# Optimization experiments

Hardware: AMD Instinct MI355X
Metric: run time of the kernel (lower is better)

## Reference

```python
import jax, jax.numpy as jnp
import numpy as np

N_NODES = 100000
N_EDGES = 600000
IN_DIM, HID_DIM, OUT_DIM = 128, 128, 128
NEG_SLOPE = 0.2  # PyG GATConv default


def _glorot(key, shape):
    fan = sum(shape)
    lim = jnp.sqrt(6.0 / fan)
    return jax.random.uniform(key, shape, jnp.float32, -lim, lim)


def setup_inputs() -> dict:
    key = jax.random.key(0)
    ks = jax.random.split(key, 10)
    x = jax.random.normal(ks[0], (N_NODES, IN_DIM), jnp.float32)
    edge_index = jax.random.randint(ks[1], (2, N_EDGES), 0, N_NODES, jnp.int64)
    return {
        "x": x,
        "edge_index": edge_index,
        "W1": _glorot(ks[2], (IN_DIM, HID_DIM)),
        "a_src1": _glorot(ks[3], (HID_DIM,)),
        "a_dst1": _glorot(ks[4], (HID_DIM,)),
        "b1": jnp.zeros((HID_DIM,), jnp.float32),
        "W2": _glorot(ks[5], (HID_DIM, OUT_DIM)),
        "a_src2": _glorot(ks[6], (OUT_DIM,)),
        "a_dst2": _glorot(ks[7], (OUT_DIM,)),
        "b2": jnp.zeros((OUT_DIM,), jnp.float32),
    }


def _gat_conv(x, src, dst, W, a_src, a_dst, b, n_nodes):
    """Single-head PyG-style GATConv (concat=True, heads=1, with self-loops already in src/dst)."""
    h = x @ W                                   # [N, F]
    alpha_s = h @ a_src                         # [N]
    alpha_d = h @ a_dst                         # [N]
    e = jax.nn.leaky_relu(alpha_s[src] + alpha_d[dst], NEG_SLOPE)  # [E]
    # segment softmax over incoming edges of each dst node
    m = jax.lax.stop_gradient(jax.ops.segment_max(e, dst, num_segments=n_nodes))
    w = jnp.exp(e - m[dst])                     # [E]
    denom = jax.ops.segment_sum(w, dst, num_segments=n_nodes)  # [N]
    alpha = w / denom[dst]                      # [E]
    out = jax.ops.segment_sum(h[src] * alpha[:, None], dst, num_segments=n_nodes)
    return out + b


def reference(x, edge_index, W1, a_src1, a_dst1, b1, W2, a_src2, a_dst2, b2):
    n = x.shape[0]
    loop = jnp.arange(n, dtype=edge_index.dtype)
    src = jnp.concatenate([edge_index[0], loop])  # add self-loops (PyG default)
    dst = jnp.concatenate([edge_index[1], loop])
    h = jax.nn.relu(_gat_conv(x, src, dst, W1, a_src1, a_dst1, b1, n))
    out = _gat_conv(h, src, dst, W2, a_src2, a_dst2, b2, n)
    return out.mean(axis=0)  # [out_dim]
```

## Files before the change

kernel.cpp:

```cpp
#include <hip/hip_runtime.h>


#define NEG_SLOPE 0.2f

typedef __attribute__((ext_vector_type(8))) short bf16x8;
typedef __attribute__((ext_vector_type(4))) float f32x4;

__device__ __forceinline__ float leaky(float x) { return x > 0.0f ? x : NEG_SLOPE * x; }

__device__ __forceinline__ unsigned int bf16rne(float f) {
  unsigned int u = __float_as_uint(f);
  return (u + 0x7fffu + ((u >> 16) & 1u)) >> 16;
}
__device__ __forceinline__ unsigned int packbf(float a, float b) {
  return bf16rne(a) | (bf16rne(b) << 16);
}
__device__ __forceinline__ float bf_lo(unsigned int u) { return __uint_as_float(u << 16); }
__device__ __forceinline__ float bf_hi(unsigned int u) { return __uint_as_float(u & 0xffff0000u); }

__device__ __forceinline__ void accum8(float* a, float w, uint4 h) {
  a[0] += w * bf_lo(h.x); a[1] += w * bf_hi(h.x);
  a[2] += w * bf_lo(h.y); a[3] += w * bf_hi(h.y);
  a[4] += w * bf_lo(h.z); a[5] += w * bf_hi(h.z);
  a[6] += w * bf_lo(h.w); a[7] += w * bf_hi(h.w);
}

__device__ __forceinline__ float2 gat_node2(
    const uint4* __restrict__ H4, const float* __restrict__ vas,
    const float* __restrict__ vad, const int* __restrict__ fill,
    const int* __restrict__ esrcp, const int2* __restrict__ ovf,
    const int* __restrict__ ovfn, int node0, int node1, int nclamp,
    int lane, int l, float* acc0, float* acc1, float* eself_out) {
  int t0 = esrcp[(size_t)node0 * 16 + l];
  int t1 = esrcp[(size_t)node1 * 16 + l];
  int dg0 = fill[node0];
  int dg1 = fill[node1];
  float ad0 = vad[node0], ad1 = vad[node1];
  float as0 = vas[node0], as1 = vas[node1];
  uint4 hs0 = H4[(size_t)node0 * 16 + l];
  uint4 hs1 = H4[(size_t)node1 * 16 + l];
  int u0 = min(max(t0, 0), nclamp);
  int u1 = min(max(t1, 0), nclamp);
  float vs0 = vas[u0];
  float vs1 = vas[u1];
  uint4 hb0[8], hb1[8];
#pragma unroll
  for (int i = 0; i < 8; i++) {
    int ut = __shfl(u0, (lane & 48) + i, 64);
    hb0[i] = H4[(size_t)ut * 16 + l];
  }
#pragma unroll
  for (int i = 0; i < 8; i++) {
    int ut = __shfl(u1, (lane & 48) + i, 64);
    hb1[i] = H4[(size_t)ut * 16 + l];
  }
  const bool big0 = dg0 > 8, big1 = dg1 > 8;
  uint4 hc0[8];
  if (big0) {
#pragma unroll
    for (int i = 0; i < 8; i++) {
      int ut = __shfl(u0, (lane & 48) + 8 + i, 64);
      hc0[i] = H4[(size_t)ut * 16 + l];
    }
  }
  float es0 = leaky(as0 + ad0), es1 = leaky(as1 + ad1);
  float wj0 = (l < dg0) ? __expf(leaky(vs0 + ad0) - es0) : 0.f;
  float wj1 = (l < dg1) ? __expf(leaky(vs1 + ad1) - es1) : 0.f;
  float ds0 = wj0, ds1 = wj1;
#pragma unroll
  for (int o = 8; o; o >>= 1) ds0 += __shfl_xor(ds0, o, 16);
#pragma unroll
  for (int o = 8; o; o >>= 1) ds1 += __shfl_xor(ds1, o, 16);
#pragma unroll
  for (int i = 0; i < 8; i++) {
    float w = __shfl(wj0, (lane & 48) + i, 64);
    accum8(acc0, w, hb0[i]);
  }
  if (big0) {
#pragma unroll
    for (int i = 0; i < 8; i++) {
      float w = __shfl(wj0, (lane & 48) + 8 + i, 64);
      accum8(acc0, w, hc0[i]);
    }
  }
  uint4 hc1[8];
  if (big1) {
#pragma unroll
    for (int i = 0; i < 8; i++) {
      int ut = __shfl(u1, (lane & 48) + 8 + i, 64);
      hc1[i] = H4[(size_t)ut * 16 + l];
    }
  }
#pragma unroll
  for (int i = 0; i < 8; i++) {
    float w = __shfl(wj1, (lane & 48) + i, 64);
    accum8(acc1, w, hb1[i]);
  }
  if (big1) {
#pragma unroll
    for (int i = 0; i < 8; i++) {
      float w = __shfl(wj1, (lane & 48) + 8 + i, 64);
      accum8(acc1, w, hc1[i]);
    }
  }
  if (dg0 > 16 || dg1 > 16) {
    int ovn = *ovfn;
    for (int k = 0; k < ovn; k++) {
      int2 ent = ovf[k];
      if (ent.x == node0) {
        float w = __expf(leaky(vas[ent.y] + ad0) - es0);
        ds0 += w;
        accum8(acc0, w, H4[(size_t)ent.y * 16 + l]);
      }
      if (ent.x == node1) {
        float w = __expf(leaky(vas[ent.y] + ad1) - es1);
        ds1 += w;
        accum8(acc1, w, H4[(size_t)ent.y * 16 + l]);
      }
    }
  }
  accum8(acc0, 1.0f, hs0);
  accum8(acc1, 1.0f, hs1);
  eself_out[0] = es0;
  eself_out[1] = es1;
  return make_float2(1.0f / (ds0 + 1.0f), 1.0f / (ds1 + 1.0f));
}

__global__ __launch_bounds__(256) void setup_k(const float* __restrict__ W1,
                                               const float* __restrict__ W2,
                                               unsigned short* __restrict__ Wf1,
                                               unsigned short* __restrict__ Wf2,
                                               int* __restrict__ fill,
                                               int* __restrict__ esrcp,
                                               int* __restrict__ ovfn,
                                               float* __restrict__ partial,
                                               int n, int nfb) {
  const int b = blockIdx.x;
  if (b < 2) {
    const float* W = b ? W2 : W1;
    unsigned short* Wf = b ? Wf2 : Wf1;
    for (int idx = threadIdx.x; idx < 16384; idx += 256) {
      int j = idx & 7;
      int lane = (idx >> 3) & 63;
      int fid = idx >> 9;
      int ct = fid >> 2, ks = fid & 3;
      int q = lane >> 4, l15 = lane & 15;
      Wf[idx] = (unsigned short)bf16rne(W[(ks * 32 + q * 8 + j) * 128 + ct * 16 + l15]);
    }
    return;
  }
  if (b == 2) {
    for (int i = threadIdx.x; i < 64 * 128; i += 256) partial[i] = 0.f;
    if (threadIdx.x == 0) *ovfn = 0;
    return;
  }
  if (b < 3 + nfb) {
    int base = (b - 3) * 1024 + threadIdx.x * 4;
#pragma unroll
    for (int i = 0; i < 4; i++)
      if (base + i < n) fill[base + i] = 0;
    return;
  }
  size_t base = (size_t)(b - 3 - nfb) * 1024 + threadIdx.x * 4;
  size_t tot = (size_t)n * 16;
  if (base + 4 <= tot) {
    *(int4*)&esrcp[base] = make_int4(0, 0, 0, 0);
  } else {
    for (size_t i = base; i < tot; i++) esrcp[i] = 0;
  }
}

__global__ void scatter_kernel(const int* __restrict__ src, const int* __restrict__ dst,
                               int* __restrict__ fill, int* __restrict__ esrcp,
                               int2* __restrict__ ovf, int* __restrict__ ovfn, int E) {
  int e = blockIdx.x * 256 + threadIdx.x;
  if (e < E) {
    int v = dst[e];
    int sv = src[e];
    int p = atomicAdd(&fill[v], 1);
    if (p < 16) {
      esrcp[(size_t)v * 16 + p] = sv;
    } else {
      int k = atomicAdd(ovfn, 1);
      ovf[k] = make_int2(v, sv);
    }
  }
}

__device__ __forceinline__ void cvt_f32(const float4* raw, bf16x8* xf) {
#pragma unroll
  for (int ks = 0; ks < 4; ks++) {
    union { bf16x8 v; unsigned int u[4]; } cv;
    cv.u[0] = packbf(raw[2 * ks].x, raw[2 * ks].y);
    cv.u[1] = packbf(raw[2 * ks].z, raw[2 * ks].w);
    cv.u[2] = packbf(raw[2 * ks + 1].x, raw[2 * ks + 1].y);
    cv.u[3] = packbf(raw[2 * ks + 1].z, raw[2 * ks + 1].w);
    xf[ks] = cv.v;
  }
}

__device__ __forceinline__ void mfma_tile(const unsigned short* WL, const bf16x8* xf,
                                          const float* __restrict__ a_s,
                                          const float* __restrict__ a_d,
                                          unsigned short* __restrict__ H,
                                          float* __restrict__ vas,
                                          float* __restrict__ vad, int myrow, bool act,
                                          int lane, int q) {
  f32x4 acc[8];
#pragma unroll
  for (int ct = 0; ct < 8; ct++) acc[ct] = (f32x4){0.f, 0.f, 0.f, 0.f};
#pragma unroll
  for (int ks = 0; ks < 4; ks++) {
    bf16x8 wf[8];
#pragma unroll
    for (int ct = 0; ct < 8; ct++)
      wf[ct] = *(const bf16x8*)&WL[(((ct << 2) + ks) << 9) + lane * 8];
#pragma unroll
    for (int ct = 0; ct < 8; ct++)
      acc[ct] = __builtin_amdgcn_mfma_f32_16x16x32_bf16(wf[ct], xf[ks], acc[ct], 0, 0, 0);
  }
  float ds = 0.f, dd = 0.f;
#pragma unroll
  for (int ct = 0; ct < 8; ct++) {
    const int c0 = ct * 16 + q * 4;
    float4 as4 = *(const float4*)&a_s[c0];
    float4 ad4 = *(const float4*)&a_d[c0];
    ds += acc[ct][0] * as4.x + acc[ct][1] * as4.y + acc[ct][2] * as4.z + acc[ct][3] * as4.w;
    dd += acc[ct][0] * ad4.x + acc[ct][1] * ad4.y + acc[ct][2] * ad4.z + acc[ct][3] * ad4.w;
    if (act) {
      uint2 o;
      o.x = packbf(acc[ct][0], acc[ct][1]);
      o.y = packbf(acc[ct][2], acc[ct][3]);
      *(uint2*)&H[(size_t)myrow * 128 + c0] = o;
    }
  }
  ds += __shfl_xor(ds, 16, 64);
  ds += __shfl_xor(ds, 32, 64);
  dd += __shfl_xor(dd, 16, 64);
  dd += __shfl_xor(dd, 32, 64);
  if (q == 0 && act) {
    vas[myrow] = ds;
    vad[myrow] = dd;
  }
}

__global__ __launch_bounds__(256) void gemm_mfma1(const float* __restrict__ Xf,
                                                  const unsigned short* __restrict__ Wf,
                                                  const float* __restrict__ a_s,
                                                  const float* __restrict__ a_d,
                                                  unsigned short* __restrict__ H,
                                                  float* __restrict__ vas,
                                                  float* __restrict__ vad, int n,
                                                  int nt16, int ngemm) {
  __shared__ unsigned short WL[32 * 512];
  const int lane = threadIdx.x & 63;
  const int wv = threadIdx.x >> 6;
  const int l15 = lane & 15;
  const int q = lane >> 4;
  const int t0 = blockIdx.x * 4 + wv;
  const int t1 = t0 + ngemm * 4;
  const int r0 = t0 * 16 + l15;
  const int r1 = t1 * 16 + l15;
  const bool wact0 = t0 < nt16;
  const bool wact1 = t1 < nt16;
  const bool act0 = wact0 && (r0 < n);
  const bool act1 = wact1 && (r1 < n);

  float4 raw0[8];
  if (wact0) {
#pragma unroll
    for (int ks = 0; ks < 4; ks++) {
      float4 z = {0.f, 0.f, 0.f, 0.f};
      raw0[2 * ks] = z;
      raw0[2 * ks + 1] = z;
      if (act0) {
        raw0[2 * ks] = *(const float4*)&Xf[(size_t)r0 * 128 + ks * 32 + q * 8];
        raw0[2 * ks + 1] = *(const float4*)&Xf[(size_t)r0 * 128 + ks * 32 + q * 8 + 4];
      }
    }
  }
  {
    const uint4* __restrict__ Wg4 = (const uint4*)Wf;
    uint4* WL4 = (uint4*)WL;
#pragma unroll
    for (int j = 0; j < 8; j++) WL4[threadIdx.x + 256 * j] = Wg4[threadIdx.x + 256 * j];
  }
  __syncthreads();
  if (!wact0) return;

  float4 raw1[8];
  if (wact1) {
#pragma unroll
    for (int ks = 0; ks < 4; ks++) {
      float4 z = {0.f, 0.f, 0.f, 0.f};
      raw1[2 * ks] = z;
      raw1[2 * ks + 1] = z;
      if (act1) {
        raw1[2 * ks] = *(const float4*)&Xf[(size_t)r1 * 128 + ks * 32 + q * 8];
        raw1[2 * ks + 1] = *(const float4*)&Xf[(size_t)r1 * 128 + ks * 32 + q * 8 + 4];
      }
    }
  }

  bf16x8 xf[4];
  cvt_f32(raw0, xf);
  mfma_tile(WL, xf, a_s, a_d, H, vas, vad, r0, act0, lane, q);
  if (wact1) {
    cvt_f32(raw1, xf);
    mfma_tile(WL, xf, a_s, a_d, H, vas, vad, r1, act1, lane, q);
  }
}

__global__ __launch_bounds__(256, 3) void agg1_gemm2(
    const unsigned short* __restrict__ HA, const float* __restrict__ vas1,
    const float* __restrict__ vad1, const int* __restrict__ fill,
    const int* __restrict__ esrcp, const int2* __restrict__ ovf,
    const int* __restrict__ ovfn, const float* __restrict__ b1,
    const unsigned short* __restrict__ Wf2, const float* __restrict__ a_s2,
    const float* __restrict__ a_d2, unsigned short* __restrict__ HB,
    float* __restrict__ vas2, float* __restrict__ vad2, int n) {
  __shared__ unsigned short Atile[32 * 128];
  __shared__ float sdot[2][2][4][16];
  const int tid = threadIdx.x;
  const int lane = tid & 63;
  const int wv = tid >> 6;
  const int q = lane >> 4;
  const int l = lane & 15;
  const int row = wv * 4 + q;
  const int base = blockIdx.x * 32;
  const int node0 = base + row;
  const int node1 = base + row + 16;
  const bool valid0 = node0 < n, valid1 = node1 < n;
  const int n0s = valid0 ? node0 : n - 1;
  const int n1s = valid1 ? node1 : n - 1;
  const uint4* __restrict__ H4 = (const uint4*)HA;

  float acc0[8], acc1[8];
#pragma unroll
  for (int k = 0; k < 8; k++) { acc0[k] = 0.f; acc1[k] = 0.f; }
  float es[2];
  float2 inv = gat_node2(H4, vas1, vad1, fill, esrcp, ovf, ovfn, n0s, n1s, n - 1,
                         lane, l, acc0, acc1, es);

  float4 b0 = *(const float4*)&b1[8 * l];
  float4 b1v = *(const float4*)&b1[8 * l + 4];
  uint4 o0 = {0u, 0u, 0u, 0u}, o1 = {0u, 0u, 0u, 0u};
  if (valid0) {
    float r0_ = fmaxf(acc0[0] * inv.x + b0.x, 0.f), r1_ = fmaxf(acc0[1] * inv.x + b0.y, 0.f);
    float r2_ = fmaxf(acc0[2] * inv.x + b0.z, 0.f), r3_ = fmaxf(acc0[3] * inv.x + b0.w, 0.f);
    float r4_ = fmaxf(acc0[4] * inv.x + b1v.x, 0.f), r5_ = fmaxf(acc0[5] * inv.x + b1v.y, 0.f);
    float r6_ = fmaxf(acc0[6] * inv.x + b1v.z, 0.f), r7_ = fmaxf(acc0[7] * inv.x + b1v.w, 0.f);
    o0.x = packbf(r0_, r1_); o0.y = packbf(r2_, r3_);
    o0.z = packbf(r4_, r5_); o0.w = packbf(r6_, r7_);
  }
  if (valid1) {
    float r0_ = fmaxf(acc1[0] * inv.y + b0.x, 0.f), r1_ = fmaxf(acc1[1] * inv.y + b0.y, 0.f);
    float r2_ = fmaxf(acc1[2] * inv.y + b0.z, 0.f), r3_ = fmaxf(acc1[3] * inv.y + b0.w, 0.f);
    float r4_ = fmaxf(acc1[4] * inv.y + b1v.x, 0.f), r5_ = fmaxf(acc1[5] * inv.y + b1v.y, 0.f);
    float r6_ = fmaxf(acc1[6] * inv.y + b1v.z, 0.f), r7_ = fmaxf(acc1[7] * inv.y + b1v.w, 0.f);
    o1.x = packbf(r0_, r1_); o1.y = packbf(r2_, r3_);
    o1.z = packbf(r4_, r5_); o1.w = packbf(r6_, r7_);
  }
  *(uint4*)&Atile[row * 128 + ((l ^ (row & 7)) << 3)] = o0;
  *(uint4*)&Atile[(row + 16) * 128 + ((l ^ (row & 7)) << 3)] = o1;
  __syncthreads();

  const int ct0 = 2 * wv, ct1 = 2 * wv + 1;
  f32x4 aA0 = {0.f, 0.f, 0.f, 0.f}, aB0 = aA0, aA1 = aA0, aB1 = aA0;
#pragma unroll
  for (int ks = 0; ks < 4; ks++) {
    bf16x8 w0 = *(const bf16x8*)&Wf2[(((ct0 << 2) + ks) << 9) + lane * 8];
    bf16x8 w1 = *(const bf16x8*)&Wf2[(((ct1 << 2) + ks) << 9) + lane * 8];
    bf16x8 x0 = *(const bf16x8*)&Atile[l * 128 + ((((ks << 2) + q) ^ (l & 7)) << 3)];
    bf16x8 x1 = *(const bf16x8*)&Atile[(16 + l) * 128 + ((((ks << 2) + q) ^ (l & 7)) << 3)];
    aA0 = __builtin_amdgcn_mfma_f32_16x16x32_bf16(w0, x0, aA0, 0, 0, 0);
    aB0 = __builtin_amdgcn_mfma_f32_16x16x32_bf16(w1, x0, aB0, 0, 0, 0);
    aA1 = __builtin_amdgcn_mfma_f32_16x16x32_bf16(w0, x1, aA1, 0, 0, 0);
    aB1 = __builtin_amdgcn_mfma_f32_16x16x32_bf16(w1, x1, aB1, 0, 0, 0);
  }

#pragma unroll
  for (int t = 0; t < 2; t++) {
    f32x4 aA = t ? aA1 : aA0;
    f32x4 aB = t ? aB1 : aB0;
    const int myrow = base + t * 16 + l;
    const bool ract = myrow < n;
    float ds = 0.f, dd = 0.f;
    {
      const int c0 = ct0 * 16 + q * 4;
      float4 as4 = *(const float4*)&a_s2[c0];
      float4 ad4 = *(const float4*)&a_d2[c0];
      ds += aA[0] * as4.x + aA[1] * as4.y + aA[2] * as4.z + aA[3] * as4.w;
      dd += aA[0] * ad4.x + aA[1] * ad4.y + aA[2] * ad4.z + aA[3] * ad4.w;
      if (ract) {
        uint2 ov;
        ov.x = packbf(aA[0], aA[1]);
        ov.y = packbf(aA[2], aA[3]);
        *(uint2*)&HB[(size_t)myrow * 128 + c0] = ov;
      }
    }
    {
      const int c0 = ct1 * 16 + q * 4;
      float4 as4 = *(const float4*)&a_s2[c0];
      float4 ad4 = *(const float4*)&a_d2[c0];
      ds += aB[0] * as4.x + aB[1] * as4.y + aB[2] * as4.z + aB[3] * as4.w;
      dd += aB[0] * ad4.x + aB[1] * ad4.y + aB[2] * ad4.z + aB[3] * ad4.w;
      if (ract) {
        uint2 ov;
        ov.x = packbf(aB[0], aB[1]);
        ov.y = packbf(aB[2], aB[3]);
        *(uint2*)&HB[(size_t)myrow * 128 + c0] = ov;
      }
    }
    ds += __shfl_xor(ds, 16, 64);
    ds += __shfl_xor(ds, 32, 64);
    dd += __shfl_xor(dd, 16, 64);
    dd += __shfl_xor(dd, 32, 64);
    if (q == 0) {
      sdot[t][0][wv][l] = ds;
      sdot[t][1][wv][l] = dd;
    }
  }
  __syncthreads();
  if (tid < 32) {
    int t = tid >> 4, i = tid & 15;
    int nn = base + tid;
    if (nn < n) {
      vas2[nn] = sdot[t][0][0][i] + sdot[t][0][1][i] + sdot[t][0][2][i] + sdot[t][0][3][i];
      vad2[nn] = sdot[t][1][0][i] + sdot[t][1][1][i] + sdot[t][1][2][i] + sdot[t][1][3][i];
    }
  }
}

__global__ __launch_bounds__(256, 3) void gat_agg_l2(
    const unsigned short* __restrict__ H, const float* __restrict__ vas,
    const float* __restrict__ vad, const int* __restrict__ fill,
    const int* __restrict__ esrcp, const int2* __restrict__ ovf,
    const int* __restrict__ ovfn, const float* __restrict__ bias,
    float* __restrict__ partial, int n) {
  const int tid = threadIdx.x;
  const int lane = tid & 63;
  const int wv = tid >> 6;
  const int q = lane >> 4;
  const int l = lane & 15;
  const int row = wv * 4 + q;
  const int base = blockIdx.x * 32;
  const int node0 = base + row;
  const int node1 = base + row + 16;
  const bool valid0 = node0 < n, valid1 = node1 < n;
  const int n0s = valid0 ? node0 : n - 1;
  const int n1s = valid1 ? node1 : n - 1;
  const uint4* __restrict__ H4 = (const uint4*)H;

  float acc0[8], acc1[8];
#pragma unroll
  for (int k = 0; k < 8; k++) { acc0[k] = 0.f; acc1[k] = 0.f; }
  float es[2];
  float2 inv = gat_node2(H4, vas, vad, fill, esrcp, ovf, ovfn, n0s, n1s, n - 1,
                         lane, l, acc0, acc1, es);

  float4 b0 = *(const float4*)&bias[8 * l];
  float4 b1v = *(const float4*)&bias[8 * l + 4];
  float out[8];
  const float i0 = valid0 ? inv.x : 0.f;
  const float i1 = valid1 ? inv.y : 0.f;
  const float bm = (valid0 ? 1.f : 0.f) + (valid1 ? 1.f : 0.f);
  out[0] = acc0[0] * i0 + acc1[0] * i1 + bm * b0.x;
  out[1] = acc0[1] * i0 + acc1[1] * i1 + bm * b0.y;
  out[2] = acc0[2] * i0 + acc1[2] * i1 + bm * b0.z;
  out[3] = acc0[3] * i0 + acc1[3] * i1 + bm * b0.w;
  out[4] = acc0[4] * i0 + acc1[4] * i1 + bm * b1v.x;
  out[5] = acc0[5] * i0 + acc1[5] * i1 + bm * b1v.y;
  out[6] = acc0[6] * i0 + acc1[6] * i1 + bm * b1v.z;
  out[7] = acc0[7] * i0 + acc1[7] * i1 + bm * b1v.w;

#pragma unroll
  for (int k = 0; k < 8; k++) {
    out[k] += __shfl_xor(out[k], 16, 64);
    out[k] += __shfl_xor(out[k], 32, 64);
  }
  __shared__ float red[4][128];
  if (q == 0) {
#pragma unroll
    for (int k = 0; k < 8; k++) red[wv][8 * l + k] = out[k];
  }
  __syncthreads();
  if (tid < 128) {
    float sm = red[0][tid] + red[1][tid] + red[2][tid] + red[3][tid];
    atomicAdd(&partial[(blockIdx.x & 63) * 128 + tid], sm);
  }
}

__global__ void finalize_k(const float* __restrict__ partial, float* __restrict__ out,
                           float invn) {
  int c = threadIdx.x;
  float s = 0.f;
#pragma unroll 8
  for (int r = 0; r < 64; r++) s += partial[r * 128 + c];
  out[c] = s * invn;
}

extern "C" void kernel_launch(void* const* d_in, const int* in_sizes, int n_in,
                              void* d_out, int out_size, void* d_ws, size_t ws_size,
                              hipStream_t stream) {
  const float* x = (const float*)d_in[0];
  const int* ei = (const int*)d_in[1];
  const float* W1 = (const float*)d_in[2];
  const float* a_src1 = (const float*)d_in[3];
  const float* a_dst1 = (const float*)d_in[4];
  const float* b1 = (const float*)d_in[5];
  const float* W2 = (const float*)d_in[6];
  const float* a_src2 = (const float*)d_in[7];
  const float* a_dst2 = (const float*)d_in[8];
  const float* b2 = (const float*)d_in[9];
  float* out = (float*)d_out;

  const int N = in_sizes[0] / 128;
  const int E = in_sizes[1] / 2;
  const int* src = ei;
  const int* dst = ei + E;

  const size_t rowpadded = (size_t)(N + 256) * 128;

  char* p = (char*)d_ws;
  unsigned short* HA = (unsigned short*)p; p += rowpadded * 2;
  unsigned short* HB = (unsigned short*)p; p += rowpadded * 2;
  float* vas1 = (float*)p;    p += (size_t)N * 4;
  float* vad1 = (float*)p;    p += (size_t)N * 4;
  float* vas2 = (float*)p;    p += (size_t)N * 4;
  float* vad2 = (float*)p;    p += (size_t)N * 4;
  int* fill = (int*)p;        p += (size_t)N * 4;
  int* esrcp = (int*)p;       p += (size_t)N * 16 * 4;
  int2* ovf = (int2*)p;       p += (size_t)E * 8;
  int* ovfn = (int*)p;        p += 16;
  float* partial = (float*)p; p += 64 * 128 * 4;
  unsigned short* Wf1 = (unsigned short*)p; p += 16384 * 2;
  unsigned short* Wf2 = (unsigned short*)p; p += 16384 * 2;

  const int eblocks = (E + 255) / 256;
  const int nt16 = (N + 15) / 16;
  const int ngemm = (nt16 + 7) / 8;
  const int aggblocks = (N + 31) / 32;
  const int nfb = (N + 1023) / 1024;
  const int neb = (N * 16 + 1023) / 1024;

  setup_k<<<3 + nfb + neb, 256, 0, stream>>>(W1, W2, Wf1, Wf2, fill, esrcp, ovfn,
                                             partial, N, nfb);
  scatter_kernel<<<eblocks, 256, 0, stream>>>(src, dst, fill, esrcp, ovf, ovfn, E);
  gemm_mfma1<<<ngemm, 256, 0, stream>>>(x, Wf1, a_src1, a_dst1, HA, vas1, vad1, N, nt16, ngemm);
  agg1_gemm2<<<aggblocks, 256, 0, stream>>>(HA, vas1, vad1, fill, esrcp, ovf, ovfn, b1,
                                            Wf2, a_src2, a_dst2, HB, vas2, vad2, N);
  gat_agg_l2<<<aggblocks, 256, 0, stream>>>(HB, vas2, vad2, fill, esrcp, ovf, ovfn, b2,
                                            partial, N);
  finalize_k<<<1, 128, 0, stream>>>(partial, out, 1.0f / (float)N);
}
```

Before: 232.8 us.

## Replace layer-2 aggregation with per-source attention weights and weighted column sum

Because only the mean of the second layer output is needed, the layer-2 gather of neighbour feature rows is replaced by accumulating each source node's total normalized attention coefficient into a per-node weight array via atomics. A second kernel then computes a single weighted sum of HB rows, and the bias is added once in the finalizer. This removes the per-edge 128-wide feature gathers in layer 2, at the cost of scattered float atomics on the weight array and an extra launch.

```diff
diff --git a/kernel.cpp b/kernel.cpp
--- a/kernel.cpp
+++ b/kernel.cpp
@@ -30,7 +30,7 @@
     const float* __restrict__ vad, const int* __restrict__ fill,
     const int* __restrict__ esrcp, const int2* __restrict__ ovf,
     const int* __restrict__ ovfn, int node0, int node1, int nclamp,
-    int lane, int l, float* acc0, float* acc1, float* eself_out) {
+    int lane, int l, float* acc0, float* acc1) {
   int t0 = esrcp[(size_t)node0 * 16 + l];
   int t1 = esrcp[(size_t)node1 * 16 + l];
   int dg0 = fill[node0];
@@ -121,8 +121,6 @@
   }
   accum8(acc0, 1.0f, hs0);
   accum8(acc1, 1.0f, hs1);
-  eself_out[0] = es0;
-  eself_out[1] = es1;
   return make_float2(1.0f / (ds0 + 1.0f), 1.0f / (ds1 + 1.0f));
 }
 
@@ -131,6 +129,7 @@
                                                unsigned short* __restrict__ Wf1,
                                                unsigned short* __restrict__ Wf2,
                                                int* __restrict__ fill,
+                                               float* __restrict__ c,
                                                int* __restrict__ esrcp,
                                                int* __restrict__ ovfn,
                                                float* __restrict__ partial,
@@ -158,7 +157,10 @@
     int base = (b - 3) * 1024 + threadIdx.x * 4;
 #pragma unroll
     for (int i = 0; i < 4; i++)
-      if (base + i < n) fill[base + i] = 0;
+      if (base + i < n) {
+        fill[base + i] = 0;
+        c[base + i] = 0.f;
+      }
     return;
   }
   size_t base = (size_t)(b - 3 - nfb) * 1024 + threadIdx.x * 4;
@@ -338,9 +340,8 @@
   float acc0[8], acc1[8];
 #pragma unroll
   for (int k = 0; k < 8; k++) { acc0[k] = 0.f; acc1[k] = 0.f; }
-  float es[2];
   float2 inv = gat_node2(H4, vas1, vad1, fill, esrcp, ovf, ovfn, n0s, n1s, n - 1,
-                         lane, l, acc0, acc1, es);
+                         lane, l, acc0, acc1);
 
   float4 b0 = *(const float4*)&b1[8 * l];
   float4 b1v = *(const float4*)&b1[8 * l + 4];
@@ -432,72 +433,83 @@
   }
 }
 
-__global__ __launch_bounds__(256, 3) void gat_agg_l2(
-    const unsigned short* __restrict__ H, const float* __restrict__ vas,
-    const float* __restrict__ vad, const int* __restrict__ fill,
-    const int* __restrict__ esrcp, const int2* __restrict__ ovf,
-    const int* __restrict__ ovfn, const float* __restrict__ bias,
-    float* __restrict__ partial, int n) {
+__global__ __launch_bounds__(256) void attn2_k(const float* __restrict__ vas,
+                                               const float* __restrict__ vad,
+                                               const int* __restrict__ fill,
+                                               const int* __restrict__ esrcp,
+                                               const int2* __restrict__ ovf,
+                                               const int* __restrict__ ovfn,
+                                               float* __restrict__ c, int n) {
   const int tid = threadIdx.x;
   const int lane = tid & 63;
-  const int wv = tid >> 6;
-  const int q = lane >> 4;
   const int l = lane & 15;
-  const int row = wv * 4 + q;
-  const int base = blockIdx.x * 32;
-  const int node0 = base + row;
-  const int node1 = base + row + 16;
-  const bool valid0 = node0 < n, valid1 = node1 < n;
-  const int n0s = valid0 ? node0 : n - 1;
-  const int n1s = valid1 ? node1 : n - 1;
-  const uint4* __restrict__ H4 = (const uint4*)H;
-
-  float acc0[8], acc1[8];
-#pragma unroll
-  for (int k = 0; k < 8; k++) { acc0[k] = 0.f; acc1[k] = 0.f; }
-  float es[2];
-  float2 inv = gat_node2(H4, vas, vad, fill, esrcp, ovf, ovfn, n0s, n1s, n - 1,
-                         lane, l, acc0, acc1, es);
-
-  float4 b0 = *(const float4*)&bias[8 * l];
-  float4 b1v = *(const float4*)&bias[8 * l + 4];
-  float out[8];
-  const float i0 = valid0 ? inv.x : 0.f;
-  const float i1 = valid1 ? inv.y : 0.f;
-  const float bm = (valid0 ? 1.f : 0.f) + (valid1 ? 1.f : 0.f);
-  out[0] = acc0[0] * i0 + acc1[0] * i1 + bm * b0.x;
-  out[1] = acc0[1] * i0 + acc1[1] * i1 + bm * b0.y;
-  out[2] = acc0[2] * i0 + acc1[2] * i1 + bm * b0.z;
-  out[3] = acc0[3] * i0 + acc1[3] * i1 + bm * b0.w;
-  out[4] = acc0[4] * i0 + acc1[4] * i1 + bm * b1v.x;
-  out[5] = acc0[5] * i0 + acc1[5] * i1 + bm * b1v.y;
-  out[6] = acc0[6] * i0 + acc1[6] * i1 + bm * b1v.z;
-  out[7] = acc0[7] * i0 + acc1[7] * i1 + bm * b1v.w;
-
-#pragma unroll
-  for (int k = 0; k < 8; k++) {
-    out[k] += __shfl_xor(out[k], 16, 64);
-    out[k] += __shfl_xor(out[k], 32, 64);
-  }
-  __shared__ float red[4][128];
-  if (q == 0) {
-#pragma unroll
-    for (int k = 0; k < 8; k++) red[wv][8 * l + k] = out[k];
-  }
-  __syncthreads();
-  if (tid < 128) {
-    float sm = red[0][tid] + red[1][tid] + red[2][tid] + red[3][tid];
-    atomicAdd(&partial[(blockIdx.x & 63) * 128 + tid], sm);
-  }
-}
-
-__global__ void finalize_k(const float* __restrict__ partial, float* __restrict__ out,
+  const int node = (blockIdx.x * 256 + tid) >> 4;
+  if (node >= n) return;
+  int traw = esrcp[(size_t)node * 16 + l];
+  int dg = fill[node];
+  float adv = vad[node];
+  float asv = vas[node];
+  int u = min(max(traw, 0), n - 1);
+  float vsr = vas[u];
+  float es = leaky(asv + adv);
+  const int dc = min(dg, 16);
+  float w = (l < dc) ? __expf(leaky(vsr + adv) - es) : 0.f;
+  float ds = w;
+#pragma unroll
+  for (int o = 8; o; o >>= 1) ds += __shfl_xor(ds, o, 16);
+  float denom = ds + 1.0f;
+  if (dg > 16) {
+    int ovn = *ovfn;
+    float extra = 0.f;
+    for (int k = l; k < ovn; k += 16) {
+      int2 ent = ovf[k];
+      if (ent.x == node) extra += __expf(leaky(vas[ent.y] + adv) - es);
+    }
+#pragma unroll
+    for (int o = 8; o; o >>= 1) extra += __shfl_xor(extra, o, 16);
+    denom += extra;
+  }
+  const float inv = 1.0f / denom;
+  if (l < dc) atomicAdd(&c[u], w * inv);
+  if (l == 0) atomicAdd(&c[node], inv);
+  if (dg > 16) {
+    int ovn = *ovfn;
+    for (int k = l; k < ovn; k += 16) {
+      int2 ent = ovf[k];
+      if (ent.x == node) {
+        float w2 = __expf(leaky(vas[ent.y] + adv) - es);
+        atomicAdd(&c[ent.y], w2 * inv);
+      }
+    }
+  }
+}
+
+__global__ __launch_bounds__(256) void wsum_k(const unsigned short* __restrict__ HB,
+                                              const float* __restrict__ c,
+                                              float* __restrict__ partial, int n,
+                                              int nwaves) {
+  const int lane = threadIdx.x & 63;
+  const int wid = blockIdx.x * 4 + (threadIdx.x >> 6);
+  const unsigned int* __restrict__ H1 = (const unsigned int*)HB;
+  float a0 = 0.f, a1 = 0.f;
+  for (int node = wid; node < n; node += nwaves) {
+    float cv = c[node];
+    unsigned int h = H1[(size_t)node * 64 + lane];
+    a0 += cv * bf_lo(h);
+    a1 += cv * bf_hi(h);
+  }
+  atomicAdd(&partial[(wid & 63) * 128 + 2 * lane], a0);
+  atomicAdd(&partial[(wid & 63) * 128 + 2 * lane + 1], a1);
+}
+
+__global__ void finalize_k(const float* __restrict__ partial,
+                           const float* __restrict__ b2, float* __restrict__ out,
                            float invn) {
-  int c = threadIdx.x;
+  int col = threadIdx.x;
   float s = 0.f;
 #pragma unroll 8
-  for (int r = 0; r < 64; r++) s += partial[r * 128 + c];
-  out[c] = s * invn;
+  for (int r = 0; r < 64; r++) s += partial[r * 128 + col];
+  out[col] = s * invn + b2[col];
 }
 
 extern "C" void kernel_launch(void* const* d_in, const int* in_sizes, int n_in,
@@ -530,6 +542,7 @@
   float* vas2 = (float*)p;    p += (size_t)N * 4;
   float* vad2 = (float*)p;    p += (size_t)N * 4;
   int* fill = (int*)p;        p += (size_t)N * 4;
+  float* cw = (float*)p;      p += (size_t)N * 4;
   int* esrcp = (int*)p;       p += (size_t)N * 16 * 4;
   int2* ovf = (int2*)p;       p += (size_t)E * 8;
   int* ovfn = (int*)p;        p += 16;
@@ -543,14 +556,16 @@
   const int aggblocks = (N + 31) / 32;
   const int nfb = (N + 1023) / 1024;
   const int neb = (N * 16 + 1023) / 1024;
-
-  setup_k<<<3 + nfb + neb, 256, 0, stream>>>(W1, W2, Wf1, Wf2, fill, esrcp, ovfn,
+  const int a2blocks = (N + 15) / 16;
+  const int nwaves = 2048;
+
+  setup_k<<<3 + nfb + neb, 256, 0, stream>>>(W1, W2, Wf1, Wf2, fill, cw, esrcp, ovfn,
                                              partial, N, nfb);
   scatter_kernel<<<eblocks, 256, 0, stream>>>(src, dst, fill, esrcp, ovf, ovfn, E);
   gemm_mfma1<<<ngemm, 256, 0, stream>>>(x, Wf1, a_src1, a_dst1, HA, vas1, vad1, N, nt16, ngemm);
   agg1_gemm2<<<aggblocks, 256, 0, stream>>>(HA, vas1, vad1, fill, esrcp, ovf, ovfn, b1,
                                             Wf2, a_src2, a_dst2, HB, vas2, vad2, N);
-  gat_agg_l2<<<aggblocks, 256, 0, stream>>>(HB, vas2, vad2, fill, esrcp, ovf, ovfn, b2,
-                                            partial, N);
-  finalize_k<<<1, 128, 0, stream>>>(partial, out, 1.0f / (float)N);
-}
+  attn2_k<<<a2blocks, 256, 0, stream>>>(vas2, vad2, fill, esrcp, ovf, ovfn, cw, N);
+  wsum_k<<<nwaves / 4, 256, 0, stream>>>(HB, cw, partial, N, nwaves);
+  finalize_k<<<1, 128, 0, stream>>>(partial, b2, out, 1.0f / (float)N);
+}
```

Measured after the change: 260.7 us. 12.0% more time.

## Merge setup, scatter and first GEMM into one launch; fold finalize into last block

Applied to the files above, without the earlier changes.

Replaces the setup, scatter and first GEMM launches with a single front kernel. Its GEMM blocks convert W1 to bf16 directly into shared memory, one block converts W2, and the remaining blocks run the edge scatter. Zeroing of fill/partial/counters moves to a hipMemsetAsync. The esrcp zeroing is dropped by masking neighbour indices with the degree. The finalize kernel is removed and replaced by a last-block-done atomic counter in the layer-2 aggregation. The aim is to cut launch overhead and serialization between small kernels. The risk is that the GEMM blocks each redo the W1 conversion, and that the scatter and GEMM now share one grid.

```diff
diff --git a/kernel.cpp b/kernel.cpp
--- a/kernel.cpp
+++ b/kernel.cpp
@@ -30,7 +30,7 @@
     const float* __restrict__ vad, const int* __restrict__ fill,
     const int* __restrict__ esrcp, const int2* __restrict__ ovf,
     const int* __restrict__ ovfn, int node0, int node1, int nclamp,
-    int lane, int l, float* acc0, float* acc1, float* eself_out) {
+    int lane, int l, float* acc0, float* acc1) {
   int t0 = esrcp[(size_t)node0 * 16 + l];
   int t1 = esrcp[(size_t)node1 * 16 + l];
   int dg0 = fill[node0];
@@ -39,8 +39,8 @@
   float as0 = vas[node0], as1 = vas[node1];
   uint4 hs0 = H4[(size_t)node0 * 16 + l];
   uint4 hs1 = H4[(size_t)node1 * 16 + l];
-  int u0 = min(max(t0, 0), nclamp);
-  int u1 = min(max(t1, 0), nclamp);
+  int u0 = (l < dg0) ? min(max(t0, 0), nclamp) : 0;
+  int u1 = (l < dg1) ? min(max(t1, 0), nclamp) : 0;
   float vs0 = vas[u0];
   float vs1 = vas[u1];
   uint4 hb0[8], hb1[8];
@@ -121,70 +121,7 @@
   }
   accum8(acc0, 1.0f, hs0);
   accum8(acc1, 1.0f, hs1);
-  eself_out[0] = es0;
-  eself_out[1] = es1;
   return make_float2(1.0f / (ds0 + 1.0f), 1.0f / (ds1 + 1.0f));
-}
-
-__global__ __launch_bounds__(256) void setup_k(const float* __restrict__ W1,
-                                               const float* __restrict__ W2,
-                                               unsigned short* __restrict__ Wf1,
-                                               unsigned short* __restrict__ Wf2,
-                                               int* __restrict__ fill,
-                                               int* __restrict__ esrcp,
-                                               int* __restrict__ ovfn,
-                                               float* __restrict__ partial,
-                                               int n, int nfb) {
-  const int b = blockIdx.x;
-  if (b < 2) {
-    const float* W = b ? W2 : W1;
-    unsigned short* Wf = b ? Wf2 : Wf1;
-    for (int idx = threadIdx.x; idx < 16384; idx += 256) {
-      int j = idx & 7;
-      int lane = (idx >> 3) & 63;
-      int fid = idx >> 9;
-      int ct = fid >> 2, ks = fid & 3;
-      int q = lane >> 4, l15 = lane & 15;
-      Wf[idx] = (unsigned short)bf16rne(W[(ks * 32 + q * 8 + j) * 128 + ct * 16 + l15]);
-    }
-    return;
-  }
-  if (b == 2) {
-    for (int i = threadIdx.x; i < 64 * 128; i += 256) partial[i] = 0.f;
-    if (threadIdx.x == 0) *ovfn = 0;
-    return;
-  }
-  if (b < 3 + nfb) {
-    int base = (b - 3) * 1024 + threadIdx.x * 4;
-#pragma unroll
-    for (int i = 0; i < 4; i++)
-      if (base + i < n) fill[base + i] = 0;
-    return;
-  }
-  size_t base = (size_t)(b - 3 - nfb) * 1024 + threadIdx.x * 4;
-  size_t tot = (size_t)n * 16;
-  if (base + 4 <= tot) {
-    *(int4*)&esrcp[base] = make_int4(0, 0, 0, 0);
-  } else {
-    for (size_t i = base; i < tot; i++) esrcp[i] = 0;
-  }
-}
-
-__global__ void scatter_kernel(const int* __restrict__ src, const int* __restrict__ dst,
-                               int* __restrict__ fill, int* __restrict__ esrcp,
-                               int2* __restrict__ ovf, int* __restrict__ ovfn, int E) {
-  int e = blockIdx.x * 256 + threadIdx.x;
-  if (e < E) {
-    int v = dst[e];
-    int sv = src[e];
-    int p = atomicAdd(&fill[v], 1);
-    if (p < 16) {
-      esrcp[(size_t)v * 16 + p] = sv;
-    } else {
-      int k = atomicAdd(ovfn, 1);
-      ovf[k] = make_int2(v, sv);
-    }
-  }
 }
 
 __device__ __forceinline__ void cvt_f32(const float4* raw, bf16x8* xf) {
@@ -244,70 +181,100 @@
   }
 }
 
-__global__ __launch_bounds__(256) void gemm_mfma1(const float* __restrict__ Xf,
-                                                  const unsigned short* __restrict__ Wf,
-                                                  const float* __restrict__ a_s,
-                                                  const float* __restrict__ a_d,
-                                                  unsigned short* __restrict__ H,
-                                                  float* __restrict__ vas,
-                                                  float* __restrict__ vad, int n,
-                                                  int nt16, int ngemm) {
-  __shared__ unsigned short WL[32 * 512];
-  const int lane = threadIdx.x & 63;
-  const int wv = threadIdx.x >> 6;
-  const int l15 = lane & 15;
-  const int q = lane >> 4;
-  const int t0 = blockIdx.x * 4 + wv;
-  const int t1 = t0 + ngemm * 4;
-  const int r0 = t0 * 16 + l15;
-  const int r1 = t1 * 16 + l15;
-  const bool wact0 = t0 < nt16;
-  const bool wact1 = t1 < nt16;
-  const bool act0 = wact0 && (r0 < n);
-  const bool act1 = wact1 && (r1 < n);
-
-  float4 raw0[8];
-  if (wact0) {
-#pragma unroll
-    for (int ks = 0; ks < 4; ks++) {
-      float4 z = {0.f, 0.f, 0.f, 0.f};
-      raw0[2 * ks] = z;
-      raw0[2 * ks + 1] = z;
-      if (act0) {
-        raw0[2 * ks] = *(const float4*)&Xf[(size_t)r0 * 128 + ks * 32 + q * 8];
-        raw0[2 * ks + 1] = *(const float4*)&Xf[(size_t)r0 * 128 + ks * 32 + q * 8 + 4];
+__global__ __launch_bounds__(256) void front_k(
+    const float* __restrict__ Xf, const float* __restrict__ W1,
+    const float* __restrict__ W2, unsigned short* __restrict__ Wf2,
+    const int* __restrict__ src, const int* __restrict__ dst,
+    int* __restrict__ fill, int* __restrict__ esrcp, int2* __restrict__ ovf,
+    int* __restrict__ ovfn, const float* __restrict__ a_s,
+    const float* __restrict__ a_d, unsigned short* __restrict__ H,
+    float* __restrict__ vas, float* __restrict__ vad, int n, int nt16, int ngemm,
+    int E) {
+  const int b = blockIdx.x;
+  if (b < ngemm) {
+    __shared__ unsigned short WL[32 * 512];
+    const int lane = threadIdx.x & 63;
+    const int wv = threadIdx.x >> 6;
+    const int l15 = lane & 15;
+    const int q = lane >> 4;
+    const int t0 = b * 4 + wv;
+    const int t1 = t0 + ngemm * 4;
+    const int r0 = t0 * 16 + l15;
+    const int r1 = t1 * 16 + l15;
+    const bool wact0 = t0 < nt16;
+    const bool wact1 = t1 < nt16;
+    const bool act0 = wact0 && (r0 < n);
+    const bool act1 = wact1 && (r1 < n);
+
+    float4 raw0[8];
+    if (wact0) {
+#pragma unroll
+      for (int ks = 0; ks < 4; ks++) {
+        float4 z = {0.f, 0.f, 0.f, 0.f};
+        raw0[2 * ks] = z;
+        raw0[2 * ks + 1] = z;
+        if (act0) {
+          raw0[2 * ks] = *(const float4*)&Xf[(size_t)r0 * 128 + ks * 32 + q * 8];
+          raw0[2 * ks + 1] = *(const float4*)&Xf[(size_t)r0 * 128 + ks * 32 + q * 8 + 4];
+        }
       }
     }
-  }
-  {
-    const uint4* __restrict__ Wg4 = (const uint4*)Wf;
-    uint4* WL4 = (uint4*)WL;
-#pragma unroll
-    for (int j = 0; j < 8; j++) WL4[threadIdx.x + 256 * j] = Wg4[threadIdx.x + 256 * j];
-  }
-  __syncthreads();
-  if (!wact0) return;
-
-  float4 raw1[8];
-  if (wact1) {
-#pragma unroll
-    for (int ks = 0; ks < 4; ks++) {
-      float4 z = {0.f, 0.f, 0.f, 0.f};
-      raw1[2 * ks] = z;
-      raw1[2 * ks + 1] = z;
-      if (act1) {
-        raw1[2 * ks] = *(const float4*)&Xf[(size_t)r1 * 128 + ks * 32 + q * 8];
-        raw1[2 * ks + 1] = *(const float4*)&Xf[(size_t)r1 * 128 + ks * 32 + q * 8 + 4];
+    for (int idx = threadIdx.x; idx < 16384; idx += 256) {
+      int j = idx & 7;
+      int ln = (idx >> 3) & 63;
+      int fid = idx >> 9;
+      int ct = fid >> 2, ks = fid & 3;
+      int qq = ln >> 4, ll = ln & 15;
+      WL[idx] = (unsigned short)bf16rne(W1[(ks * 32 + qq * 8 + j) * 128 + ct * 16 + ll]);
+    }
+    __syncthreads();
+    if (!wact0) return;
+
+    float4 raw1[8];
+    if (wact1) {
+#pragma unroll
+      for (int ks = 0; ks < 4; ks++) {
+        float4 z = {0.f, 0.f, 0.f, 0.f};
+        raw1[2 * ks] = z;
+        raw1[2 * ks + 1] = z;
+        if (act1) {
+          raw1[2 * ks] = *(const float4*)&Xf[(size_t)r1 * 128 + ks * 32 + q * 8];
+          raw1[2 * ks + 1] = *(const float4*)&Xf[(size_t)r1 * 128 + ks * 32 + q * 8 + 4];
+        }
       }
     }
-  }
-
-  bf16x8 xf[4];
-  cvt_f32(raw0, xf);
-  mfma_tile(WL, xf, a_s, a_d, H, vas, vad, r0, act0, lane, q);
-  if (wact1) {
-    cvt_f32(raw1, xf);
-    mfma_tile(WL, xf, a_s, a_d, H, vas, vad, r1, act1, lane, q);
+
+    bf16x8 xf[4];
+    cvt_f32(raw0, xf);
+    mfma_tile(WL, xf, a_s, a_d, H, vas, vad, r0, act0, lane, q);
+    if (wact1) {
+      cvt_f32(raw1, xf);
+      mfma_tile(WL, xf, a_s, a_d, H, vas, vad, r1, act1, lane, q);
+    }
+    return;
+  }
+  if (b == ngemm) {
+    for (int idx = threadIdx.x; idx < 16384; idx += 256) {
+      int j = idx & 7;
+      int ln = (idx >> 3) & 63;
+      int fid = idx >> 9;
+      int ct = fid >> 2, ks = fid & 3;
+      int qq = ln >> 4, ll = ln & 15;
+      Wf2[idx] = (unsigned short)bf16rne(W2[(ks * 32 + qq * 8 + j) * 128 + ct * 16 + ll]);
+    }
+    return;
+  }
+  int e = (b - ngemm - 1) * 256 + threadIdx.x;
+  if (e < E) {
+    int v = dst[e];
+    int sv = src[e];
+    int p = atomicAdd(&fill[v], 1);
+    if (p < 16) {
+      esrcp[(size_t)v * 16 + p] = sv;
+    } else {
+      int k = atomicAdd(ovfn, 1);
+      ovf[k] = make_int2(v, sv);
+    }
   }
 }
 
@@ -338,9 +305,8 @@
   float acc0[8], acc1[8];
 #pragma unroll
   for (int k = 0; k < 8; k++) { acc0[k] = 0.f; acc1[k] = 0.f; }
-  float es[2];
   float2 inv = gat_node2(H4, vas1, vad1, fill, esrcp, ovf, ovfn, n0s, n1s, n - 1,
-                         lane, l, acc0, acc1, es);
+                         lane, l, acc0, acc1);
 
   float4 b0 = *(const float4*)&b1[8 * l];
   float4 b1v = *(const float4*)&b1[8 * l + 4];
@@ -437,7 +403,8 @@
     const float* __restrict__ vad, const int* __restrict__ fill,
     const int* __restrict__ esrcp, const int2* __restrict__ ovf,
     const int* __restrict__ ovfn, const float* __restrict__ bias,
-    float* __restrict__ partial, int n) {
+    float* __restrict__ partial, float* __restrict__ out, int* __restrict__ done,
+    int n, float invn) {
   const int tid = threadIdx.x;
   const int lane = tid & 63;
   const int wv = tid >> 6;
@@ -455,49 +422,55 @@
   float acc0[8], acc1[8];
 #pragma unroll
   for (int k = 0; k < 8; k++) { acc0[k] = 0.f; acc1[k] = 0.f; }
-  float es[2];
   float2 inv = gat_node2(H4, vas, vad, fill, esrcp, ovf, ovfn, n0s, n1s, n - 1,
-                         lane, l, acc0, acc1, es);
+                         lane, l, acc0, acc1);
 
   float4 b0 = *(const float4*)&bias[8 * l];
   float4 b1v = *(const float4*)&bias[8 * l + 4];
-  float out[8];
+  float o[8];
   const float i0 = valid0 ? inv.x : 0.f;
   const float i1 = valid1 ? inv.y : 0.f;
   const float bm = (valid0 ? 1.f : 0.f) + (valid1 ? 1.f : 0.f);
-  out[0] = acc0[0] * i0 + acc1[0] * i1 + bm * b0.x;
-  out[1] = acc0[1] * i0 + acc1[1] * i1 + bm * b0.y;
-  out[2] = acc0[2] * i0 + acc1[2] * i1 + bm * b0.z;
-  out[3] = acc0[3] * i0 + acc1[3] * i1 + bm * b0.w;
-  out[4] = acc0[4] * i0 + acc1[4] * i1 + bm * b1v.x;
-  out[5] = acc0[5] * i0 + acc1[5] * i1 + bm * b1v.y;
-  out[6] = acc0[6] * i0 + acc1[6] * i1 + bm * b1v.z;
-  out[7] = acc0[7] * i0 + acc1[7] * i1 + bm * b1v.w;
+  o[0] = acc0[0] * i0 + acc1[0] * i1 + bm * b0.x;
+  o[1] = acc0[1] * i0 + acc1[1] * i1 + bm * b0.y;
+  o[2] = acc0[2] * i0 + acc1[2] * i1 + bm * b0.z;
+  o[3] = acc0[3] * i0 + acc1[3] * i1 + bm * b0.w;
+  o[4] = acc0[4] * i0 + acc1[4] * i1 + bm * b1v.x;
+  o[5] = acc0[5] * i0 + acc1[5] * i1 + bm * b1v.y;
+  o[6] = acc0[6] * i0 + acc1[6] * i1 + bm * b1v.z;
+  o[7] = acc0[7] * i0 + acc1[7] * i1 + bm * b1v.w;
 
 #pragma unroll
   for (int k = 0; k < 8; k++) {
-    out[k] += __shfl_xor(out[k], 16, 64);
-    out[k] += __shfl_xor(out[k], 32, 64);
+    o[k] += __shfl_xor(o[k], 16, 64);
+    o[k] += __shfl_xor(o[k], 32, 64);
   }
   __shared__ float red[4][128];
   if (q == 0) {
 #pragma unroll
-    for (int k = 0; k < 8; k++) red[wv][8 * l + k] = out[k];
+    for (int k = 0; k < 8; k++) red[wv][8 * l + k] = o[k];
   }
   __syncthreads();
   if (tid < 128) {
     float sm = red[0][tid] + red[1][tid] + red[2][tid] + red[3][tid];
     atomicAdd(&partial[(blockIdx.x & 63) * 128 + tid], sm);
   }
-}
-
-__global__ void finalize_k(const float* __restrict__ partial, float* __restrict__ out,
-                           float invn) {
-  int c = threadIdx.x;
-  float s = 0.f;
+  __syncthreads();
+
+  __shared__ int islast;
+  if (tid == 0) {
+    int v = __hip_atomic_fetch_add(done, 1, __ATOMIC_ACQ_REL, __HIP_MEMORY_SCOPE_AGENT);
+    islast = (v == (int)gridDim.x - 1) ? 1 : 0;
+  }
+  __syncthreads();
+  if (islast && tid < 128) {
+    float s = 0.f;
 #pragma unroll 8
-  for (int r = 0; r < 64; r++) s += partial[r * 128 + c];
-  out[c] = s * invn;
+    for (int r = 0; r < 64; r++)
+      s += __hip_atomic_load(&partial[r * 128 + tid], __ATOMIC_RELAXED,
+                             __HIP_MEMORY_SCOPE_AGENT);
+    out[tid] = s * invn;
+  }
 }
 
 extern "C" void kernel_launch(void* const* d_in, const int* in_sizes, int n_in,
@@ -523,34 +496,38 @@
   const size_t rowpadded = (size_t)(N + 256) * 128;
 
   char* p = (char*)d_ws;
-  unsigned short* HA = (unsigned short*)p; p += rowpadded * 2;
-  unsigned short* HB = (unsigned short*)p; p += rowpadded * 2;
-  float* vas1 = (float*)p;    p += (size_t)N * 4;
-  float* vad1 = (float*)p;    p += (size_t)N * 4;
-  float* vas2 = (float*)p;    p += (size_t)N * 4;
-  float* vad2 = (float*)p;    p += (size_t)N * 4;
-  int* fill = (int*)p;        p += (size_t)N * 4;
-  int* esrcp = (int*)p;       p += (size_t)N * 16 * 4;
-  int2* ovf = (int2*)p;       p += (size_t)E * 8;
-  int* ovfn = (int*)p;        p += 16;
-  float* partial = (float*)p; p += 64 * 128 * 4;
-  unsigned short* Wf1 = (unsigned short*)p; p += 16384 * 2;
-  unsigned short* Wf2 = (unsigned short*)p; p += 16384 * 2;
+  auto carve = [&p](size_t bytes) {
+    char* r = p;
+    p += (bytes + 255) & ~(size_t)255;
+    return r;
+  };
+  unsigned short* HA = (unsigned short*)carve(rowpadded * 2);
+  unsigned short* HB = (unsigned short*)carve(rowpadded * 2);
+  char* zstart = p;
+  int* fill = (int*)carve((size_t)N * 4);
+  float* partial = (float*)carve(64 * 128 * 4);
+  int* done = (int*)carve(256);
+  int* ovfn = (int*)carve(256);
+  const size_t zsize = (size_t)(p - zstart);
+  float* vas1 = (float*)carve((size_t)N * 4);
+  float* vad1 = (float*)carve((size_t)N * 4);
+  float* vas2 = (float*)carve((size_t)N * 4);
+  float* vad2 = (float*)carve((size_t)N * 4);
+  int* esrcp = (int*)carve((size_t)N * 16 * 4);
+  int2* ovf = (int2*)carve((size_t)E * 8);
+  unsigned short* Wf2 = (unsigned short*)carve(16384 * 2);
 
   const int eblocks = (E + 255) / 256;
   const int nt16 = (N + 15) / 16;
   const int ngemm = (nt16 + 7) / 8;
   const int aggblocks = (N + 31) / 32;
-  const int nfb = (N + 1023) / 1024;
-  const int neb = (N * 16 + 1023) / 1024;
-
-  setup_k<<<3 + nfb + neb, 256, 0, stream>>>(W1, W2, Wf1, Wf2, fill, esrcp, ovfn,
-                                             partial, N, nfb);
-  scatter_kernel<<<eblocks, 256, 0, stream>>>(src, dst, fill, esrcp, ovf, ovfn, E);
-  gemm_mfma1<<<ngemm, 256, 0, stream>>>(x, Wf1, a_src1, a_dst1, HA, vas1, vad1, N, nt16, ngemm);
+
+  hipMemsetAsync(zstart, 0, zsize, stream);
+  front_k<<<ngemm + 1 + eblocks, 256, 0, stream>>>(
+      x, W1, W2, Wf2, src, dst, fill, esrcp, ovf, ovfn, a_src1, a_dst1, HA, vas1,
+      vad1, N, nt16, ngemm, E);
   agg1_gemm2<<<aggblocks, 256, 0, stream>>>(HA, vas1, vad1, fill, esrcp, ovf, ovfn, b1,
                                             Wf2, a_src2, a_dst2, HB, vas2, vad2, N);
   gat_agg_l2<<<aggblocks, 256, 0, stream>>>(HB, vas2, vad2, fill, esrcp, ovf, ovfn, b2,
-                                            partial, N);
-  finalize_k<<<1, 128, 0, stream>>>(partial, out, 1.0f / (float)N);
-}
+                                            partial, out, done, N, 1.0f / (float)N);
+}
```

Result: slower. 318.3 us (+36.8%).
